# Performance work log

Hardware: AMD Instinct MI355X
Metric: run time of the kernel (lower is better)

Reference implementation:

```python
import jax, jax.numpy as jnp
import numpy as np

DIM = 128
HEADS = 4
WIN = (2, 7, 7)
SHIFT = (1, 3, 3)
B, D, H, W = 8, 8, 56, 56
LN_EPS = 1e-5


def _rel_pos_index(ws):
    # static (N, N) int index into the relative position bias table
    coords = np.stack(np.meshgrid(np.arange(ws[0]), np.arange(ws[1]), np.arange(ws[2]), indexing='ij'))
    cf = coords.reshape(3, -1)
    rel = (cf[:, :, None] - cf[:, None, :]).transpose(1, 2, 0)  # (N, N, 3)
    rel[:, :, 0] += ws[0] - 1
    rel[:, :, 1] += ws[1] - 1
    rel[:, :, 2] += ws[2] - 1
    rel[:, :, 0] *= (2 * ws[1] - 1) * (2 * ws[2] - 1)
    rel[:, :, 1] *= 2 * ws[2] - 1
    return rel.sum(-1)


_REL_IDX = _rel_pos_index(WIN)  # (98, 98)


def _layernorm(x, g, b):
    m = x.mean(-1, keepdims=True)
    v = ((x - m) ** 2).mean(-1, keepdims=True)
    return (x - m) * jax.lax.rsqrt(v + LN_EPS) * g + b


def _forward(x, mask_matrix, norm1_g, norm1_b, qkv_w, qkv_b, rel_bias,
             proj_w, proj_b, norm2_g, norm2_b, fc1_w, fc1_b, fc2_w, fc2_b):
    Bx, Dx, Hx, Wx, C = x.shape
    wd, wh, ww = WIN
    sd, sh, sw = SHIFT
    N = wd * wh * ww
    hd = C // HEADS

    shortcut = x
    h = _layernorm(x, norm1_g, norm1_b)
    # cyclic shift (D, H, W divisible by window -> no padding needed)
    h = jnp.roll(h, (-sd, -sh, -sw), axis=(1, 2, 3))
    # window partition -> (B_, N, C)
    xw = h.reshape(Bx, Dx // wd, wd, Hx // wh, wh, Wx // ww, ww, C)
    xw = xw.transpose(0, 1, 3, 5, 2, 4, 6, 7).reshape(-1, N, C)
    B_ = xw.shape[0]

    qkv = xw @ qkv_w.T + qkv_b  # (B_, N, 3C)
    qkv = qkv.reshape(B_, N, 3, HEADS, hd).transpose(2, 0, 3, 1, 4)  # (3, B_, h, N, hd)
    q = qkv[0] * (hd ** -0.5)
    k = qkv[1]
    v = qkv[2]

    attn = jnp.einsum('bhnd,bhmd->bhnm', q, k)  # (B_, h, N, N)
    bias = rel_bias[_REL_IDX.reshape(-1)].reshape(N, N, HEADS).transpose(2, 0, 1)
    attn = attn + bias[None]
    nW = mask_matrix.shape[0]
    attn = attn.reshape(B_ // nW, nW, HEADS, N, N) + mask_matrix[None, :, None]
    attn = jax.nn.softmax(attn.reshape(B_, HEADS, N, N), axis=-1)

    out = jnp.einsum('bhnm,bhmd->bnhd', attn, v).reshape(B_, N, C)
    out = out @ proj_w.T + proj_b
    # window reverse -> (B, D, H, W, C)
    out = out.reshape(Bx, Dx // wd, Hx // wh, Wx // ww, wd, wh, ww, C)
    out = out.transpose(0, 1, 4, 2, 5, 3, 6, 7).reshape(Bx, Dx, Hx, Wx, C)
    out = jnp.roll(out, (sd, sh, sw), axis=(1, 2, 3))

    x = shortcut + out
    y = _layernorm(x, norm2_g, norm2_b)
    y = jax.nn.gelu(y @ fc1_w.T + fc1_b, approximate=False)
    y = y @ fc2_w.T + fc2_b
    return x + y


def setup_inputs():
    key = jax.random.key(0)
    ks = jax.random.split(key, 6)
    C = DIM
    wd, wh, ww = WIN
    x = jax.random.normal(ks[0], (B, D, H, W, C), jnp.float32)

    # shifted-window attention mask (standard Video-Swin compute_mask)
    img_mask = np.zeros((1, D, H, W, 1), np.float32)
    cnt = 0
    sl = lambda w, s: (slice(0, -w), slice(-w, -s), slice(-s, None))
    for d in sl(WIN[0], SHIFT[0]):
        for h in sl(WIN[1], SHIFT[1]):
            for w in sl(WIN[2], SHIFT[2]):
                img_mask[:, d, h, w, :] = cnt
                cnt += 1
    mw = img_mask.reshape(1, D // wd, wd, H // wh, wh, W // ww, ww, 1)
    mw = mw.transpose(0, 1, 3, 5, 2, 4, 6, 7).reshape(-1, wd * wh * ww)  # (nW, N)
    am = mw[:, None, :] - mw[:, :, None]
    mask_matrix = jnp.asarray(np.where(am != 0, -100.0, 0.0).astype(np.float32))

    nbias = (2 * wd - 1) * (2 * wh - 1) * (2 * ww - 1)
    p = lambda k, shape: jax.random.normal(k, shape, jnp.float32) * 0.02
    return {
        'x': x, 'mask_matrix': mask_matrix,
        'norm1_g': jnp.ones((C,), jnp.float32), 'norm1_b': jnp.zeros((C,), jnp.float32),
        'qkv_w': p(ks[1], (3 * C, C)), 'qkv_b': jnp.zeros((3 * C,), jnp.float32),
        'rel_bias': p(ks[2], (nbias, HEADS)),
        'proj_w': p(ks[3], (C, C)), 'proj_b': jnp.zeros((C,), jnp.float32),
        'norm2_g': jnp.ones((C,), jnp.float32), 'norm2_b': jnp.zeros((C,), jnp.float32),
        'fc1_w': p(ks[4], (4 * C, C)), 'fc1_b': jnp.zeros((4 * C,), jnp.float32),
        'fc2_w': p(ks[5], (C, 4 * C)), 'fc2_b': jnp.zeros((C,), jnp.float32),
    }


def reference(x, mask_matrix, norm1_g, norm1_b, qkv_w, qkv_b, rel_bias,
              proj_w, proj_b, norm2_g, norm2_b, fc1_w, fc1_b, fc2_w, fc2_b):
    return _forward(x, mask_matrix, norm1_g, norm1_b, qkv_w, qkv_b, rel_bias,
                    proj_w, proj_b, norm2_g, norm2_b, fc1_w, fc1_b, fc2_w, fc2_b)
```

## Files before the change

kernel.cpp:

```cpp
#include <hip/hip_runtime.h>
#include <hip/hip_bf16.h>

#define C_DIM 128
#define N_WIN 98
#define M_TOK 200704
#define B_WIN 2048

struct __align__(8) bf16x4 { __hip_bfloat16 h[4]; };

typedef __attribute__((ext_vector_type(8))) short bf16x8_t;
typedef __attribute__((ext_vector_type(4))) float f32x4_t;

__device__ __forceinline__ int token_spatial_index(int row) {
    int widx = row / 98;
    int n = row - widx * 98;
    int b   = widx >> 8;
    int rem = widx & 255;
    int dI = rem >> 6;
    int hI = (rem >> 3) & 7;
    int wI = rem & 7;
    int dw = n / 49;
    int r49 = n - dw * 49;
    int hw = r49 / 7;
    int ww = r49 - hw * 7;
    int d = dI * 2 + dw;
    int h = hI * 7 + hw;
    int w = wI * 7 + ww;
    d = (d + 1) & 7;
    h += 3; if (h >= 56) h -= 56;
    w += 3; if (w >= 56) w -= 56;
    return ((b * 8 + d) * 56 + h) * 56 + w;
}

__global__ __launch_bounds__(256) void ln1_qkv_kernel(
    const float* __restrict__ x,
    const float* __restrict__ g1,
    const float* __restrict__ b1,
    const float* __restrict__ qkv_w,
    const float* __restrict__ qkv_b,
    __hip_bfloat16* __restrict__ qkv_out)
{
    __shared__ __align__(16) __hip_bfloat16 Abf[64][136];
    __shared__ __align__(16) __hip_bfloat16 Wbf[192][136];
    __shared__ int srcL[64];

    const int tid  = threadIdx.x;
    const int lane = tid & 63;
    const int wv   = tid >> 6;
    const int rowbase = blockIdx.x * 64;

    if (tid < 64) srcL[tid] = token_spatial_index(rowbase + tid);
    __syncthreads();

    {
        int r = tid >> 2, part = tid & 3;
        const float* xp = x + (size_t)srcL[r] * 128 + part * 32;
        float v[32];
        float s = 0.f, ss = 0.f;
        #pragma unroll
        for (int j = 0; j < 8; ++j) {
            float4 f = *(const float4*)(xp + j * 4);
            v[j*4+0] = f.x; v[j*4+1] = f.y; v[j*4+2] = f.z; v[j*4+3] = f.w;
            s  += f.x + f.y + f.z + f.w;
            ss += f.x*f.x + f.y*f.y + f.z*f.z + f.w*f.w;
        }
        s += __shfl_xor(s, 1); ss += __shfl_xor(ss, 1);
        s += __shfl_xor(s, 2); ss += __shfl_xor(ss, 2);
        float m = s * (1.f / 128.f);
        float var = ss * (1.f / 128.f) - m * m;
        float rstd = rsqrtf(var + 1e-5f);
        #pragma unroll
        for (int j = 0; j < 8; ++j) {
            int k = part * 32 + j * 4;
            bf16x4 pk;
            pk.h[0] = __float2bfloat16((v[j*4+0] - m) * rstd * g1[k+0] + b1[k+0]);
            pk.h[1] = __float2bfloat16((v[j*4+1] - m) * rstd * g1[k+1] + b1[k+1]);
            pk.h[2] = __float2bfloat16((v[j*4+2] - m) * rstd * g1[k+2] + b1[k+2]);
            pk.h[3] = __float2bfloat16((v[j*4+3] - m) * rstd * g1[k+3] + b1[k+3]);
            *(bf16x4*)(&Abf[r][k]) = pk;
        }
    }
    __syncthreads();

    const int lm = lane & 15, quad = lane >> 4;
    const int rw = wv * 16;

    bf16x8_t xfr[4];
    #pragma unroll
    for (int s = 0; s < 4; ++s)
        xfr[s] = *(const bf16x8_t*)(&Abf[rw + lm][s * 32 + quad * 8]);

    for (int nt = 0; nt < 2; ++nt) {
        #pragma unroll
        for (int i = 0; i < 24; ++i) {
            int e = tid + i * 256;
            int c = e >> 5, kq = e & 31;
            float4 f = *(const float4*)(qkv_w + (size_t)(nt * 192 + c) * 128 + kq * 4);
            bf16x4 pk;
            pk.h[0] = __float2bfloat16(f.x); pk.h[1] = __float2bfloat16(f.y);
            pk.h[2] = __float2bfloat16(f.z); pk.h[3] = __float2bfloat16(f.w);
            *(bf16x4*)(&Wbf[c][kq * 4]) = pk;
        }
        __syncthreads();

        for (int ct = 0; ct < 12; ++ct) {
            f32x4_t acc = {0.f, 0.f, 0.f, 0.f};
            #pragma unroll
            for (int s = 0; s < 4; ++s) {
                bf16x8_t wfr = *(const bf16x8_t*)(&Wbf[ct * 16 + lm][s * 32 + quad * 8]);
                acc = __builtin_amdgcn_mfma_f32_16x16x32_bf16(wfr, xfr[s], acc, 0, 0, 0);
            }
            int grow = rowbase + rw + lm;
            int gcol = nt * 192 + ct * 16 + quad * 4;
            float4 bb = *(const float4*)(qkv_b + gcol);
            bf16x4 pk;
            pk.h[0] = __float2bfloat16(acc[0] + bb.x);
            pk.h[1] = __float2bfloat16(acc[1] + bb.y);
            pk.h[2] = __float2bfloat16(acc[2] + bb.z);
            pk.h[3] = __float2bfloat16(acc[3] + bb.w);
            *(bf16x4*)(qkv_out + (size_t)grow * 384 + gcol) = pk;
        }
        __syncthreads();
    }
}

#define SWZ(r, c) (((r) * 128) + ((c) ^ (((r) & 7) << 3)))

__global__ __launch_bounds__(256) void attn_mfma_kernel(
    __hip_bfloat16* __restrict__ qkv,
    const float* __restrict__ rel_bias)
{
    __shared__ __align__(16) __hip_bfloat16 Kb[112][40];
    __shared__ __align__(16) __hip_bfloat16 Vt[32 * 128];
    __shared__ __align__(16) __hip_bfloat16 Pb[112 * 128];
    __shared__ float biasL[507];
    __shared__ int   idnL[98];
    __shared__ int   nbL[98];

    const int tid  = threadIdx.x;
    const int lane = tid & 63;
    const int wv   = tid >> 6;
    const int widx = blockIdx.x >> 2;
    const int head = blockIdx.x & 3;
    const int co   = head * 32;
    const size_t base = (size_t)widx * 98 * 384;

    bf16x8_t zz = {};
    for (int e = tid; e < 448; e += 256) {
        int row = e >> 2, c8 = e & 3;
        if (row < 98) {
            *(bf16x8_t*)(&Kb[row][c8 * 8]) =
                *(const bf16x8_t*)(qkv + base + (size_t)row * 384 + 128 + co + c8 * 8);
        } else {
            *(bf16x8_t*)(&Kb[row][c8 * 8]) = zz;
        }
    }
    for (int e = tid; e < 448; e += 256) {
        int row = e >> 2, c8 = e & 3;
        if (row < 98) {
            bf16x8_t v = *(const bf16x8_t*)(qkv + base + (size_t)row * 384 + 256 + co + c8 * 8);
            #pragma unroll
            for (int j = 0; j < 8; ++j) Vt[SWZ(c8 * 8 + j, row)] = ((__hip_bfloat16*)&v)[j];
        }
    }
    for (int e = tid; e < 1024; e += 256) {
        int r = e >> 5, c = 96 + (e & 31);
        if (c >= 98) Vt[SWZ(r, c)] = __float2bfloat16(0.f);
    }
    for (int e = tid; e < 1792; e += 256) {
        int r = e >> 4, c = 112 + (e & 15);
        Pb[SWZ(r, c)] = __float2bfloat16(0.f);
    }
    for (int i = tid; i < 507; i += 256) biasL[i] = rel_bias[i * 4 + head];
    if (tid < 98) {
        int n = tid;
        int dw = n / 49, r49 = n - dw * 49, hw = r49 / 7, ww2 = r49 - hw * 7;
        nbL[n] = dw * 169 + hw * 13 + ww2;
        int wloc = widx & 255;
        int dI = wloc >> 6, hI = (wloc >> 3) & 7, wI = wloc & 7;
        int d = dI * 2 + dw, h = hI * 7 + hw, w = wI * 7 + ww2;
        int di = (d < 6) ? 0 : (d < 7 ? 1 : 2);
        int hi = (h < 49) ? 0 : (h < 52 ? 1 : 2);
        int wi = (w < 49) ? 0 : (w < 52 ? 1 : 2);
        idnL[n] = di * 9 + hi * 3 + wi;
    }
    __syncthreads();

    const int lm = lane & 15, quad = lane >> 4;
    const float scale = 0.17677669529663687f;

    int  mnb[7], mid[7];
    bool mok[7];
    #pragma unroll
    for (int tN = 0; tN < 7; ++tN) {
        int m = tN * 16 + lm;
        mok[tN] = (m < 98);
        mnb[tN] = mok[tN] ? nbL[m] : 0;
        mid[tN] = mok[tN] ? idnL[m] : -1;
    }

    for (int tM = wv; tM < 7; tM += 4) {
        int qrow = tM * 16 + lm;
        bf16x8_t afr = zz;
        if (qrow < 98)
            afr = *(const bf16x8_t*)(qkv + base + (size_t)qrow * 384 + co + quad * 8);
        f32x4_t acc[7];
        #pragma unroll
        for (int tN = 0; tN < 7; ++tN) {
            bf16x8_t bfr = *(const bf16x8_t*)(&Kb[tN * 16 + lm][quad * 8]);
            f32x4_t c0 = {0.f, 0.f, 0.f, 0.f};
            acc[tN] = __builtin_amdgcn_mfma_f32_16x16x32_bf16(afr, bfr, c0, 0, 0, 0);
        }
        int  nnb[4], nid[4];
        bool nok[4];
        #pragma unroll
        for (int rg = 0; rg < 4; ++rg) {
            int n = tM * 16 + quad * 4 + rg;
            nok[rg] = (n < 98);
            nnb[rg] = nok[rg] ? nbL[n] : 0;
            nid[rg] = nok[rg] ? idnL[n] : -2;
        }
        float sv[7][4];
        #pragma unroll
        for (int tN = 0; tN < 7; ++tN) {
            #pragma unroll
            for (int rg = 0; rg < 4; ++rg) {
                float s;
                if (nok[rg] && mok[tN]) {
                    s = acc[tN][rg] * scale + biasL[nnb[rg] - mnb[tN] + 253];
                    s += (nid[rg] == mid[tN]) ? 0.f : -100.f;
                } else {
                    s = -1e30f;
                }
                sv[tN][rg] = s;
            }
        }
        #pragma unroll
        for (int rg = 0; rg < 4; ++rg) {
            float mx = sv[0][rg];
            #pragma unroll
            for (int tN = 1; tN < 7; ++tN) mx = fmaxf(mx, sv[tN][rg]);
            mx = fmaxf(mx, __shfl_xor(mx, 1));
            mx = fmaxf(mx, __shfl_xor(mx, 2));
            mx = fmaxf(mx, __shfl_xor(mx, 4));
            mx = fmaxf(mx, __shfl_xor(mx, 8));
            float p[7], sum = 0.f;
            #pragma unroll
            for (int tN = 0; tN < 7; ++tN) { p[tN] = __expf(sv[tN][rg] - mx); sum += p[tN]; }
            sum += __shfl_xor(sum, 1);
            sum += __shfl_xor(sum, 2);
            sum += __shfl_xor(sum, 4);
            sum += __shfl_xor(sum, 8);
            float inv = 1.f / sum;
            int n = tM * 16 + quad * 4 + rg;
            #pragma unroll
            for (int tN = 0; tN < 7; ++tN)
                Pb[SWZ(n, tN * 16 + lm)] = __float2bfloat16(p[tN] * inv);
        }
    }
    __syncthreads();

    for (int t = wv; t < 14; t += 4) {
        int tM = t >> 1, tN = t & 1;
        f32x4_t acc = {0.f, 0.f, 0.f, 0.f};
        #pragma unroll
        for (int s = 0; s < 4; ++s) {
            bf16x8_t afr = *(const bf16x8_t*)(&Pb[SWZ(tM * 16 + lm, s * 32 + quad * 8)]);
            bf16x8_t bfr = *(const bf16x8_t*)(&Vt[SWZ(tN * 16 + lm, s * 32 + quad * 8)]);
            acc = __builtin_amdgcn_mfma_f32_16x16x32_bf16(afr, bfr, acc, 0, 0, 0);
        }
        int m = tN * 16 + lm;
        #pragma unroll
        for (int rg = 0; rg < 4; ++rg) {
            int n = tM * 16 + quad * 4 + rg;
            if (n < 98)
                qkv[base + (size_t)n * 384 + co + m] = __float2bfloat16(acc[rg]);
        }
    }
}

__global__ __launch_bounds__(256) void proj_kernel(
    const __hip_bfloat16* __restrict__ attn,
    const float* __restrict__ proj_w,
    const float* __restrict__ proj_b,
    const float* __restrict__ x,
    float* __restrict__ x2)
{
    __shared__ __align__(16) __hip_bfloat16 Abf[64][136];
    __shared__ __align__(16) __hip_bfloat16 Wbf[128][136];
    __shared__ int dstL[64];

    const int tid  = threadIdx.x;
    const int lane = tid & 63;
    const int wv   = tid >> 6;
    const int rowbase = blockIdx.x * 64;

    if (tid < 64) dstL[tid] = token_spatial_index(rowbase + tid);

    #pragma unroll
    for (int i = 0; i < 4; ++i) {
        int e = tid + i * 256;
        int r = e >> 4, c8 = e & 15;
        *(bf16x8_t*)(&Abf[r][c8 * 8]) = *(const bf16x8_t*)(attn + (size_t)(rowbase + r) * 384 + c8 * 8);
    }
    #pragma unroll
    for (int i = 0; i < 16; ++i) {
        int e = tid + i * 256;
        int c = e >> 5, kq = e & 31;
        float4 f = *(const float4*)(proj_w + (size_t)c * 128 + kq * 4);
        bf16x4 pk;
        pk.h[0] = __float2bfloat16(f.x); pk.h[1] = __float2bfloat16(f.y);
        pk.h[2] = __float2bfloat16(f.z); pk.h[3] = __float2bfloat16(f.w);
        *(bf16x4*)(&Wbf[c][kq * 4]) = pk;
    }
    __syncthreads();

    const int lm = lane & 15, quad = lane >> 4;
    const int rw = wv * 16;

    bf16x8_t xfr[4];
    #pragma unroll
    for (int s = 0; s < 4; ++s)
        xfr[s] = *(const bf16x8_t*)(&Abf[rw + lm][s * 32 + quad * 8]);

    const int dst = dstL[rw + lm];

    #pragma unroll
    for (int ct = 0; ct < 8; ++ct) {
        f32x4_t acc = {0.f, 0.f, 0.f, 0.f};
        #pragma unroll
        for (int s = 0; s < 4; ++s) {
            bf16x8_t wfr = *(const bf16x8_t*)(&Wbf[ct * 16 + lm][s * 32 + quad * 8]);
            acc = __builtin_amdgcn_mfma_f32_16x16x32_bf16(wfr, xfr[s], acc, 0, 0, 0);
        }
        int gcol = ct * 16 + quad * 4;
        float4 bb = *(const float4*)(proj_b + gcol);
        size_t off = (size_t)dst * 128 + gcol;
        float4 xr = *(const float4*)(x + off);
        float4 res;
        res.x = acc[0] + bb.x + xr.x;
        res.y = acc[1] + bb.y + xr.y;
        res.z = acc[2] + bb.z + xr.z;
        res.w = acc[3] + bb.w + xr.w;
        *(float4*)(x2 + off) = res;
    }
}

__global__ __launch_bounds__(256) void prep_weights(
    const float* __restrict__ fc1_w,
    const float* __restrict__ fc2_w,
    __hip_bfloat16* __restrict__ wb)
{
    int i = blockIdx.x * 256 + threadIdx.x;
    if (i < 65536)       wb[i] = __float2bfloat16(fc1_w[i]);
    else if (i < 131072) wb[i] = __float2bfloat16(fc2_w[i - 65536]);
}

__global__ __launch_bounds__(256, 3) void mlp_mfma_kernel(
    const float* __restrict__ x2,
    const float* __restrict__ g2,
    const float* __restrict__ b2,
    const __hip_bfloat16* __restrict__ fc1_wb,
    const __hip_bfloat16* __restrict__ fc2_wb,
    const float* __restrict__ fc1_b,
    const float* __restrict__ fc2_b,
    float* __restrict__ out)
{
    __shared__ __align__(16) __hip_bfloat16 Abf[64][136];
    __shared__ __align__(16) __hip_bfloat16 Hbf[64][264];

    const int tid  = threadIdx.x;
    const int lane = tid & 63;
    const int wv   = tid >> 6;
    const int rowbase = blockIdx.x * 64;

    {
        int r = tid >> 2, part = tid & 3;
        const float* xp = x2 + (size_t)(rowbase + r) * 128 + part * 32;
        float v[32];
        float s = 0.f, ss = 0.f;
        #pragma unroll
        for (int j = 0; j < 8; ++j) {
            float4 f = *(const float4*)(xp + j * 4);
            v[j*4+0] = f.x; v[j*4+1] = f.y; v[j*4+2] = f.z; v[j*4+3] = f.w;
            s  += f.x + f.y + f.z + f.w;
            ss += f.x*f.x + f.y*f.y + f.z*f.z + f.w*f.w;
        }
        s += __shfl_xor(s, 1); ss += __shfl_xor(ss, 1);
        s += __shfl_xor(s, 2); ss += __shfl_xor(ss, 2);
        float m = s * (1.f / 128.f);
        float var = ss * (1.f / 128.f) - m * m;
        float rstd = rsqrtf(var + 1e-5f);
        #pragma unroll
        for (int j = 0; j < 8; ++j) {
            int k = part * 32 + j * 4;
            bf16x4 pk;
            pk.h[0] = __float2bfloat16((v[j*4+0] - m) * rstd * g2[k+0] + b2[k+0]);
            pk.h[1] = __float2bfloat16((v[j*4+1] - m) * rstd * g2[k+1] + b2[k+1]);
            pk.h[2] = __float2bfloat16((v[j*4+2] - m) * rstd * g2[k+2] + b2[k+2]);
            pk.h[3] = __float2bfloat16((v[j*4+3] - m) * rstd * g2[k+3] + b2[k+3]);
            *(bf16x4*)(&Abf[r][k]) = pk;
        }
    }
    __syncthreads();

    const int lm   = lane & 15;
    const int quad = lane >> 4;

    f32x4_t acc2[2][4];
    #pragma unroll
    for (int ct = 0; ct < 2; ++ct)
        #pragma unroll
        for (int rt = 0; rt < 4; ++rt)
            acc2[ct][rt] = f32x4_t{0.f, 0.f, 0.f, 0.f};

    for (int c = 0; c < 2; ++c) {
        {
            bf16x8_t afr[4][4];
            #pragma unroll
            for (int rt = 0; rt < 4; ++rt)
                #pragma unroll
                for (int s = 0; s < 4; ++s)
                    afr[rt][s] = *(const bf16x8_t*)(&Abf[rt * 16 + lm][s * 32 + quad * 8]);

            #pragma unroll
            for (int ctb = 0; ctb < 2; ++ctb) {
                bf16x8_t wfr[2][4];
                #pragma unroll
                for (int cti = 0; cti < 2; ++cti) {
                    int hcol = c * 256 + wv * 64 + (ctb * 2 + cti) * 16 + lm;
                    const __hip_bfloat16* wp = fc1_wb + (size_t)hcol * 128 + quad * 8;
                    #pragma unroll
                    for (int s = 0; s < 4; ++s)
                        wfr[cti][s] = *(const bf16x8_t*)(wp + s * 32);
                }
                #pragma unroll
                for (int cti = 0; cti < 2; ++cti) {
                    int ct = ctb * 2 + cti;
                    int hcol = c * 256 + wv * 64 + ct * 16 + lm;
                    float bb = fc1_b[hcol];
                    f32x4_t a0 = {0.f,0.f,0.f,0.f}, a1 = {0.f,0.f,0.f,0.f};
                    f32x4_t a2 = {0.f,0.f,0.f,0.f}, a3 = {0.f,0.f,0.f,0.f};
                    #pragma unroll
                    for (int s = 0; s < 4; ++s) {
                        a0 = __builtin_amdgcn_mfma_f32_16x16x32_bf16(afr[0][s], wfr[cti][s], a0, 0, 0, 0);
                        a1 = __builtin_amdgcn_mfma_f32_16x16x32_bf16(afr[1][s], wfr[cti][s], a1, 0, 0, 0);
                        a2 = __builtin_amdgcn_mfma_f32_16x16x32_bf16(afr[2][s], wfr[cti][s], a2, 0, 0, 0);
                        a3 = __builtin_amdgcn_mfma_f32_16x16x32_bf16(afr[3][s], wfr[cti][s], a3, 0, 0, 0);
                    }
                    int lc = wv * 64 + ct * 16 + lm;
                    #pragma unroll
                    for (int rg = 0; rg < 4; ++rg) {
                        float v0 = a0[rg] + bb, v1 = a1[rg] + bb, v2 = a2[rg] + bb, v3 = a3[rg] + bb;
                        v0 = 0.5f * v0 * (1.f + erff(v0 * 0.70710678118654752f));
                        v1 = 0.5f * v1 * (1.f + erff(v1 * 0.70710678118654752f));
                        v2 = 0.5f * v2 * (1.f + erff(v2 * 0.70710678118654752f));
                        v3 = 0.5f * v3 * (1.f + erff(v3 * 0.70710678118654752f));
                        Hbf[ 0 + quad * 4 + rg][lc] = __float2bfloat16(v0);
                        Hbf[16 + quad * 4 + rg][lc] = __float2bfloat16(v1);
                        Hbf[32 + quad * 4 + rg][lc] = __float2bfloat16(v2);
                        Hbf[48 + quad * 4 + rg][lc] = __float2bfloat16(v3);
                    }
                }
            }
        }
        __syncthreads();

        {
            bf16x8_t wfr2[2][8];
            #pragma unroll
            for (int ct = 0; ct < 2; ++ct) {
                int ccol = wv * 32 + ct * 16 + lm;
                const __hip_bfloat16* wp = fc2_wb + (size_t)ccol * 512 + c * 256 + quad * 8;
                #pragma unroll
                for (int s = 0; s < 8; ++s)
                    wfr2[ct][s] = *(const bf16x8_t*)(wp + s * 32);
            }
            #pragma unroll
            for (int s = 0; s < 8; ++s) {
                bf16x8_t hfr[4];
                #pragma unroll
                for (int rt = 0; rt < 4; ++rt)
                    hfr[rt] = *(const bf16x8_t*)(&Hbf[rt * 16 + lm][s * 32 + quad * 8]);
                #pragma unroll
                for (int ct = 0; ct < 2; ++ct)
                    #pragma unroll
                    for (int rt = 0; rt < 4; ++rt)
                        acc2[ct][rt] = __builtin_amdgcn_mfma_f32_16x16x32_bf16(hfr[rt], wfr2[ct][s], acc2[ct][rt], 0, 0, 0);
            }
        }
        __syncthreads();
    }

    #pragma unroll
    for (int ct = 0; ct < 2; ++ct) {
        int ccol = wv * 32 + ct * 16 + lm;
        float bb = fc2_b[ccol];
        #pragma unroll
        for (int rt = 0; rt < 4; ++rt) {
            #pragma unroll
            for (int rg = 0; rg < 4; ++rg) {
                int rr = rt * 16 + quad * 4 + rg;
                size_t off = (size_t)(rowbase + rr) * 128 + ccol;
                out[off] = acc2[ct][rt][rg] + bb + x2[off];
            }
        }
    }
}

extern "C" void kernel_launch(void* const* d_in, const int* in_sizes, int n_in,
                              void* d_out, int out_size, void* d_ws, size_t ws_size,
                              hipStream_t stream) {
    const float* x        = (const float*)d_in[0];
    const float* n1g      = (const float*)d_in[2];
    const float* n1b      = (const float*)d_in[3];
    const float* qkv_w    = (const float*)d_in[4];
    const float* qkv_b    = (const float*)d_in[5];
    const float* rel_bias = (const float*)d_in[6];
    const float* proj_w   = (const float*)d_in[7];
    const float* proj_b   = (const float*)d_in[8];
    const float* n2g      = (const float*)d_in[9];
    const float* n2b      = (const float*)d_in[10];
    const float* fc1_w    = (const float*)d_in[11];
    const float* fc1_b    = (const float*)d_in[12];
    const float* fc2_w    = (const float*)d_in[13];
    const float* fc2_b    = (const float*)d_in[14];
    float* out = (float*)d_out;

    __hip_bfloat16* qkv = (__hip_bfloat16*)d_ws;
    float* x2 = (float*)((char*)d_ws + 154140672);
    __hip_bfloat16* wb  = (__hip_bfloat16*)d_ws;
    __hip_bfloat16* fc1_wb = wb;
    __hip_bfloat16* fc2_wb = wb + 65536;

    ln1_qkv_kernel<<<3136, 256, 0, stream>>>(x, n1g, n1b, qkv_w, qkv_b, qkv);
    attn_mfma_kernel<<<8192, 256, 0, stream>>>(qkv, rel_bias);
    proj_kernel<<<3136, 256, 0, stream>>>(qkv, proj_w, proj_b, x, x2);
    prep_weights<<<512, 256, 0, stream>>>(fc1_w, fc2_w, wb);
    mlp_mfma_kernel<<<3136, 256, 0, stream>>>(x2, n2g, n2b, fc1_wb, fc2_wb, fc1_b, fc2_b, out);
}
```

Measured before the change: 611.5 us.

## Pre-convert QKV and proj weights to bf16 and stream them from global into registers

Adds a small kernel that converts qkv_w and proj_w to bf16 once, using the output buffer as scratch. The QKV and projection GEMM kernels no longer stage fp32 weights into a large LDS tile per block. Instead each wave loads its own weight column slice straight from global into registers, and each block computes all 64 rows by reusing A fragments. This removes the per-block fp32->bf16 conversion and the LDS weight footprint so more blocks fit per CU (launch bounds 3). The cost is more global and L2 weight traffic per wave and higher register pressure.

```diff
diff --git a/kernel.cpp b/kernel.cpp
--- a/kernel.cpp
+++ b/kernel.cpp
@@ -32,16 +32,25 @@
     return ((b * 8 + d) * 56 + h) * 56 + w;
 }
 
-__global__ __launch_bounds__(256) void ln1_qkv_kernel(
+__global__ __launch_bounds__(256) void prep_qp_weights(
+    const float* __restrict__ qkv_w,
+    const float* __restrict__ proj_w,
+    __hip_bfloat16* __restrict__ qp)
+{
+    int i = blockIdx.x * 256 + threadIdx.x;
+    if (i < 49152)      qp[i] = __float2bfloat16(qkv_w[i]);
+    else if (i < 65536) qp[i] = __float2bfloat16(proj_w[i - 49152]);
+}
+
+__global__ __launch_bounds__(256, 3) void ln1_qkv_kernel(
     const float* __restrict__ x,
     const float* __restrict__ g1,
     const float* __restrict__ b1,
-    const float* __restrict__ qkv_w,
+    const __hip_bfloat16* __restrict__ qkv_wb,
     const float* __restrict__ qkv_b,
     __hip_bfloat16* __restrict__ qkv_out)
 {
     __shared__ __align__(16) __hip_bfloat16 Abf[64][136];
-    __shared__ __align__(16) __hip_bfloat16 Wbf[192][136];
     __shared__ int srcL[64];
 
     const int tid  = threadIdx.x;
@@ -82,45 +91,63 @@
     }
     __syncthreads();
 
-    const int lm = lane & 15, quad = lane >> 4;
-    const int rw = wv * 16;
-
-    bf16x8_t xfr[4];
-    #pragma unroll
-    for (int s = 0; s < 4; ++s)
-        xfr[s] = *(const bf16x8_t*)(&Abf[rw + lm][s * 32 + quad * 8]);
-
-    for (int nt = 0; nt < 2; ++nt) {
-        #pragma unroll
-        for (int i = 0; i < 24; ++i) {
-            int e = tid + i * 256;
-            int c = e >> 5, kq = e & 31;
-            float4 f = *(const float4*)(qkv_w + (size_t)(nt * 192 + c) * 128 + kq * 4);
+    const int lm   = lane & 15;
+    const int quad = lane >> 4;
+    const int colbase = wv * 96;
+
+    bf16x8_t afr[4][4];
+    #pragma unroll
+    for (int rt = 0; rt < 4; ++rt)
+        #pragma unroll
+        for (int s = 0; s < 4; ++s)
+            afr[rt][s] = *(const bf16x8_t*)(&Abf[rt * 16 + lm][s * 32 + quad * 8]);
+
+    #pragma unroll
+    for (int ctb = 0; ctb < 3; ++ctb) {
+        bf16x8_t wfr[2][4];
+        #pragma unroll
+        for (int cti = 0; cti < 2; ++cti) {
+            int wcol = colbase + (ctb * 2 + cti) * 16 + lm;
+            const __hip_bfloat16* wp = qkv_wb + (size_t)wcol * 128 + quad * 8;
+            #pragma unroll
+            for (int s = 0; s < 4; ++s)
+                wfr[cti][s] = *(const bf16x8_t*)(wp + s * 32);
+        }
+        #pragma unroll
+        for (int cti = 0; cti < 2; ++cti) {
+            int gcol4 = colbase + (ctb * 2 + cti) * 16 + quad * 4;
+            float4 fb = *(const float4*)(qkv_b + gcol4);
+            f32x4_t a0 = {0.f,0.f,0.f,0.f}, a1 = {0.f,0.f,0.f,0.f};
+            f32x4_t a2 = {0.f,0.f,0.f,0.f}, a3 = {0.f,0.f,0.f,0.f};
+            #pragma unroll
+            for (int s = 0; s < 4; ++s) {
+                a0 = __builtin_amdgcn_mfma_f32_16x16x32_bf16(wfr[cti][s], afr[0][s], a0, 0, 0, 0);
+                a1 = __builtin_amdgcn_mfma_f32_16x16x32_bf16(wfr[cti][s], afr[1][s], a1, 0, 0, 0);
+                a2 = __builtin_amdgcn_mfma_f32_16x16x32_bf16(wfr[cti][s], afr[2][s], a2, 0, 0, 0);
+                a3 = __builtin_amdgcn_mfma_f32_16x16x32_bf16(wfr[cti][s], afr[3][s], a3, 0, 0, 0);
+            }
             bf16x4 pk;
-            pk.h[0] = __float2bfloat16(f.x); pk.h[1] = __float2bfloat16(f.y);
-            pk.h[2] = __float2bfloat16(f.z); pk.h[3] = __float2bfloat16(f.w);
-            *(bf16x4*)(&Wbf[c][kq * 4]) = pk;
-        }
-        __syncthreads();
-
-        for (int ct = 0; ct < 12; ++ct) {
-            f32x4_t acc = {0.f, 0.f, 0.f, 0.f};
-            #pragma unroll
-            for (int s = 0; s < 4; ++s) {
-                bf16x8_t wfr = *(const bf16x8_t*)(&Wbf[ct * 16 + lm][s * 32 + quad * 8]);
-                acc = __builtin_amdgcn_mfma_f32_16x16x32_bf16(wfr, xfr[s], acc, 0, 0, 0);
-            }
-            int grow = rowbase + rw + lm;
-            int gcol = nt * 192 + ct * 16 + quad * 4;
-            float4 bb = *(const float4*)(qkv_b + gcol);
-            bf16x4 pk;
-            pk.h[0] = __float2bfloat16(acc[0] + bb.x);
-            pk.h[1] = __float2bfloat16(acc[1] + bb.y);
-            pk.h[2] = __float2bfloat16(acc[2] + bb.z);
-            pk.h[3] = __float2bfloat16(acc[3] + bb.w);
-            *(bf16x4*)(qkv_out + (size_t)grow * 384 + gcol) = pk;
-        }
-        __syncthreads();
+            pk.h[0] = __float2bfloat16(a0[0] + fb.x);
+            pk.h[1] = __float2bfloat16(a0[1] + fb.y);
+            pk.h[2] = __float2bfloat16(a0[2] + fb.z);
+            pk.h[3] = __float2bfloat16(a0[3] + fb.w);
+            *(bf16x4*)(qkv_out + (size_t)(rowbase +  0 + lm) * 384 + gcol4) = pk;
+            pk.h[0] = __float2bfloat16(a1[0] + fb.x);
+            pk.h[1] = __float2bfloat16(a1[1] + fb.y);
+            pk.h[2] = __float2bfloat16(a1[2] + fb.z);
+            pk.h[3] = __float2bfloat16(a1[3] + fb.w);
+            *(bf16x4*)(qkv_out + (size_t)(rowbase + 16 + lm) * 384 + gcol4) = pk;
+            pk.h[0] = __float2bfloat16(a2[0] + fb.x);
+            pk.h[1] = __float2bfloat16(a2[1] + fb.y);
+            pk.h[2] = __float2bfloat16(a2[2] + fb.z);
+            pk.h[3] = __float2bfloat16(a2[3] + fb.w);
+            *(bf16x4*)(qkv_out + (size_t)(rowbase + 32 + lm) * 384 + gcol4) = pk;
+            pk.h[0] = __float2bfloat16(a3[0] + fb.x);
+            pk.h[1] = __float2bfloat16(a3[1] + fb.y);
+            pk.h[2] = __float2bfloat16(a3[2] + fb.z);
+            pk.h[3] = __float2bfloat16(a3[3] + fb.w);
+            *(bf16x4*)(qkv_out + (size_t)(rowbase + 48 + lm) * 384 + gcol4) = pk;
+        }
     }
 }
 
@@ -279,15 +306,14 @@
     }
 }
 
-__global__ __launch_bounds__(256) void proj_kernel(
+__global__ __launch_bounds__(256, 3) void proj_kernel(
     const __hip_bfloat16* __restrict__ attn,
-    const float* __restrict__ proj_w,
+    const __hip_bfloat16* __restrict__ proj_wb,
     const float* __restrict__ proj_b,
     const float* __restrict__ x,
     float* __restrict__ x2)
 {
     __shared__ __align__(16) __hip_bfloat16 Abf[64][136];
-    __shared__ __align__(16) __hip_bfloat16 Wbf[128][136];
     __shared__ int dstL[64];
 
     const int tid  = threadIdx.x;
@@ -303,46 +329,55 @@
         int r = e >> 4, c8 = e & 15;
         *(bf16x8_t*)(&Abf[r][c8 * 8]) = *(const bf16x8_t*)(attn + (size_t)(rowbase + r) * 384 + c8 * 8);
     }
-    #pragma unroll
-    for (int i = 0; i < 16; ++i) {
-        int e = tid + i * 256;
-        int c = e >> 5, kq = e & 31;
-        float4 f = *(const float4*)(proj_w + (size_t)c * 128 + kq * 4);
-        bf16x4 pk;
-        pk.h[0] = __float2bfloat16(f.x); pk.h[1] = __float2bfloat16(f.y);
-        pk.h[2] = __float2bfloat16(f.z); pk.h[3] = __float2bfloat16(f.w);
-        *(bf16x4*)(&Wbf[c][kq * 4]) = pk;
-    }
     __syncthreads();
 
-    const int lm = lane & 15, quad = lane >> 4;
-    const int rw = wv * 16;
-
-    bf16x8_t xfr[4];
-    #pragma unroll
-    for (int s = 0; s < 4; ++s)
-        xfr[s] = *(const bf16x8_t*)(&Abf[rw + lm][s * 32 + quad * 8]);
-
-    const int dst = dstL[rw + lm];
-
-    #pragma unroll
-    for (int ct = 0; ct < 8; ++ct) {
-        f32x4_t acc = {0.f, 0.f, 0.f, 0.f};
+    const int lm   = lane & 15;
+    const int quad = lane >> 4;
+    const int colbase = wv * 32;
+
+    bf16x8_t afr[4][4];
+    #pragma unroll
+    for (int rt = 0; rt < 4; ++rt)
+        #pragma unroll
+        for (int s = 0; s < 4; ++s)
+            afr[rt][s] = *(const bf16x8_t*)(&Abf[rt * 16 + lm][s * 32 + quad * 8]);
+
+    bf16x8_t wfr[2][4];
+    #pragma unroll
+    for (int cti = 0; cti < 2; ++cti) {
+        int wcol = colbase + cti * 16 + lm;
+        const __hip_bfloat16* wp = proj_wb + (size_t)wcol * 128 + quad * 8;
+        #pragma unroll
+        for (int s = 0; s < 4; ++s)
+            wfr[cti][s] = *(const bf16x8_t*)(wp + s * 32);
+    }
+
+    #pragma unroll
+    for (int cti = 0; cti < 2; ++cti) {
+        int gcol4 = colbase + cti * 16 + quad * 4;
+        float4 fb = *(const float4*)(proj_b + gcol4);
+        f32x4_t a0 = {0.f,0.f,0.f,0.f}, a1 = {0.f,0.f,0.f,0.f};
+        f32x4_t a2 = {0.f,0.f,0.f,0.f}, a3 = {0.f,0.f,0.f,0.f};
         #pragma unroll
         for (int s = 0; s < 4; ++s) {
-            bf16x8_t wfr = *(const bf16x8_t*)(&Wbf[ct * 16 + lm][s * 32 + quad * 8]);
-            acc = __builtin_amdgcn_mfma_f32_16x16x32_bf16(wfr, xfr[s], acc, 0, 0, 0);
-        }
-        int gcol = ct * 16 + quad * 4;
-        float4 bb = *(const float4*)(proj_b + gcol);
-        size_t off = (size_t)dst * 128 + gcol;
-        float4 xr = *(const float4*)(x + off);
-        float4 res;
-        res.x = acc[0] + bb.x + xr.x;
-        res.y = acc[1] + bb.y + xr.y;
-        res.z = acc[2] + bb.z + xr.z;
-        res.w = acc[3] + bb.w + xr.w;
-        *(float4*)(x2 + off) = res;
+            a0 = __builtin_amdgcn_mfma_f32_16x16x32_bf16(wfr[cti][s], afr[0][s], a0, 0, 0, 0);
+            a1 = __builtin_amdgcn_mfma_f32_16x16x32_bf16(wfr[cti][s], afr[1][s], a1, 0, 0, 0);
+            a2 = __builtin_amdgcn_mfma_f32_16x16x32_bf16(wfr[cti][s], afr[2][s], a2, 0, 0, 0);
+            a3 = __builtin_amdgcn_mfma_f32_16x16x32_bf16(wfr[cti][s], afr[3][s], a3, 0, 0, 0);
+        }
+        f32x4_t ar[4] = {a0, a1, a2, a3};
+        #pragma unroll
+        for (int rt = 0; rt < 4; ++rt) {
+            int dst = dstL[rt * 16 + lm];
+            size_t off = (size_t)dst * 128 + gcol4;
+            float4 xr = *(const float4*)(x + off);
+            float4 res;
+            res.x = ar[rt][0] + fb.x + xr.x;
+            res.y = ar[rt][1] + fb.y + xr.y;
+            res.z = ar[rt][2] + fb.z + xr.z;
+            res.w = ar[rt][3] + fb.w + xr.w;
+            *(float4*)(x2 + off) = res;
+        }
     }
 }
 
@@ -533,9 +568,14 @@
     __hip_bfloat16* fc1_wb = wb;
     __hip_bfloat16* fc2_wb = wb + 65536;
 
-    ln1_qkv_kernel<<<3136, 256, 0, stream>>>(x, n1g, n1b, qkv_w, qkv_b, qkv);
+    __hip_bfloat16* qp_wb   = (__hip_bfloat16*)d_out;
+    __hip_bfloat16* qkv_wb  = qp_wb;
+    __hip_bfloat16* proj_wb = qp_wb + 49152;
+
+    prep_qp_weights<<<256, 256, 0, stream>>>(qkv_w, proj_w, qp_wb);
+    ln1_qkv_kernel<<<3136, 256, 0, stream>>>(x, n1g, n1b, qkv_wb, qkv_b, qkv);
     attn_mfma_kernel<<<8192, 256, 0, stream>>>(qkv, rel_bias);
-    proj_kernel<<<3136, 256, 0, stream>>>(qkv, proj_w, proj_b, x, x2);
+    proj_kernel<<<3136, 256, 0, stream>>>(qkv, proj_wb, proj_b, x, x2);
     prep_weights<<<512, 256, 0, stream>>>(fc1_w, fc2_w, wb);
     mlp_mfma_kernel<<<3136, 256, 0, stream>>>(x2, n2g, n2b, fc1_wb, fc2_wb, fc1_b, fc2_b, out);
 }
```

Measured after the change: 610.5 us. No clear change (-0.2%).
